# Optimization experiments

Measured on AMD Instinct MI355X. Metric: run time of the kernel, lower is better.

## Reference

```python
import jax, jax.numpy as jnp
import numpy as np

N_NODES = 100000
N_EDGES = 1600000
NUM_FEATURES = 128
HIDDEN = 128


def _linear_init(key, fan_in, fan_out):
    kw, kb = jax.random.split(key)
    bound = 1.0 / np.sqrt(fan_in)
    w = jax.random.uniform(kw, (fan_in, fan_out), jnp.float32, -bound, bound)
    b = jax.random.uniform(kb, (fan_out,), jnp.float32, -bound, bound)
    return w, b


def setup_inputs() -> dict:
    key = jax.random.key(0)
    ks = jax.random.split(key, 8)
    x = jax.random.normal(ks[0], (N_NODES, NUM_FEATURES), jnp.float32)
    edge_index = jax.random.randint(ks[1], (2, N_EDGES), 0, N_NODES, jnp.int64)
    w11, b11 = _linear_init(ks[2], NUM_FEATURES, HIDDEN)
    w12, b12 = _linear_init(ks[3], HIDDEN, HIDDEN)
    w21, b21 = _linear_init(ks[4], HIDDEN, HIDDEN)
    w22, b22 = _linear_init(ks[5], HIDDEN, HIDDEN)
    w31, b31 = _linear_init(ks[6], HIDDEN, HIDDEN)
    w32, b32 = _linear_init(ks[7], HIDDEN, 1)
    return {"x": x, "edge_index": edge_index,
            "w11": w11, "b11": b11, "w12": w12, "b12": b12,
            "w21": w21, "b21": b21, "w22": w22, "b22": b22,
            "w31": w31, "b31": b31, "w32": w32, "b32": b32}


def _gin_conv(x, src, dst, w1, b1, w2, b2):
    # GINConv (eps=0): h_i = MLP(x_i + sum_{j->i} x_j)
    agg = jax.ops.segment_sum(x[src], dst, num_segments=N_NODES)
    h = x + agg
    h = jax.nn.relu(h @ w1 + b1)
    return h @ w2 + b2


def reference(x, edge_index, w11, b11, w12, b12, w21, b21, w22, b22, w31, b31, w32, b32):
    src, dst = edge_index[0], edge_index[1]
    h = _gin_conv(x, src, dst, w11, b11, w12, b12)
    h = _gin_conv(h, src, dst, w21, b21, w22, b22)
    h = _gin_conv(h, src, dst, w31, b31, w32, b32)  # [N, 1]
    return h
```

## Files before the change

kernel.cpp:

```cpp
#include <hip/hip_runtime.h>

#define NN 100000
#define NE 1600000
#define F 128
#define NBUCK ((NN + 255) >> 8)
#define EPB (NE / 256)

typedef _Float16 f16x8 __attribute__((ext_vector_type(8)));
typedef float    f32x4 __attribute__((ext_vector_type(4)));
typedef unsigned short ushort8v __attribute__((ext_vector_type(8)));
typedef unsigned short ushort4v __attribute__((ext_vector_type(4)));

__device__ inline unsigned short f2h(float f) {
    _Float16 h = (_Float16)f;
    return __builtin_bit_cast(unsigned short, h);
}
__device__ inline float h2f(unsigned short u) {
    return (float)__builtin_bit_cast(_Float16, u);
}

__global__ __launch_bounds__(256) void k_bhist(const int* __restrict__ dst, int* __restrict__ bcnt) {
    __shared__ int sc[NBUCK];
    for (int i = threadIdx.x; i < NBUCK; i += 256) sc[i] = 0;
    __syncthreads();
    int stride = gridDim.x * 256;
    for (int e = blockIdx.x * 256 + threadIdx.x; e < NE; e += stride)
        atomicAdd(&sc[dst[e] >> 8], 1);
    __syncthreads();
    for (int i = threadIdx.x; i < NBUCK; i += 256) {
        int c = sc[i];
        if (c) atomicAdd(&bcnt[i], c);
    }
}

__global__ void k_bscan(const int* __restrict__ bcnt, int* __restrict__ bbase, int* __restrict__ bcur) {
    __shared__ int s[512];
    int t = threadIdx.x;
    int v = (t < NBUCK) ? bcnt[t] : 0;
    s[t] = v;
    __syncthreads();
    for (int off = 1; off < 512; off <<= 1) {
        int u = (t >= off) ? s[t - off] : 0;
        __syncthreads();
        s[t] += u;
        __syncthreads();
    }
    int excl = s[t] - v;
    if (t < NBUCK) { bbase[t] = excl; bcur[t] = excl; }
    if (t == 0) bbase[NBUCK] = NE;
}

__global__ __launch_bounds__(256) void k_scatterA(const int* __restrict__ src,
                                                  const int* __restrict__ dst,
                                                  int* __restrict__ bcur,
                                                  unsigned* __restrict__ scratch) {
    __shared__ uint2 sEdge[EPB];
    __shared__ int cnt[512];
    __shared__ int scn[512];
    __shared__ int cntB[512];
    __shared__ int gbase[512];
    __shared__ int ssum[256];

    const int tid = threadIdx.x;
    const int ebase = blockIdx.x * EPB;

#pragma unroll
    for (int i = tid; i < 512; i += 256) { cnt[i] = 0; cntB[i] = 0; }
    __syncthreads();

    for (int i = tid; i < EPB; i += 256) {
        int b = dst[ebase + i] >> 8;
        atomicAdd(&cnt[b], 1);
    }
    __syncthreads();

    int c0 = cnt[2 * tid], c1 = cnt[2 * tid + 1];
    ssum[tid] = c0 + c1;
    __syncthreads();
    for (int off = 1; off < 256; off <<= 1) {
        int v = (tid >= off) ? ssum[tid - off] : 0;
        __syncthreads();
        ssum[tid] += v;
        __syncthreads();
    }
    int texcl = (tid == 0) ? 0 : ssum[tid - 1];
    scn[2 * tid] = texcl;
    scn[2 * tid + 1] = texcl + c0;
#pragma unroll
    for (int i = tid; i < NBUCK; i += 256) {
        int c = cnt[i];
        gbase[i] = c ? atomicAdd(&bcur[i], c) : 0;
    }
    __syncthreads();

    for (int i = tid; i < EPB; i += 256) {
        int s = src[ebase + i], d = dst[ebase + i];
        int b = d >> 8;
        int rank = atomicAdd(&cntB[b], 1);
        sEdge[scn[b] + rank] = make_uint2((unsigned)s, (unsigned)d);
    }
    __syncthreads();

    for (int i = tid; i < EPB; i += 256) {
        uint2 ed = sEdge[i];
        int b = (int)(ed.y >> 8);
        unsigned w = ((ed.y & 255u) << 24) | ed.x;
        scratch[gbase[b] + (i - scn[b])] = w;
    }
}

__global__ __launch_bounds__(256) void k_fillB(const int* __restrict__ bbase,
                                               const unsigned* __restrict__ scratch,
                                               int* __restrict__ row_ptr,
                                               int* __restrict__ csr) {
    __shared__ int cnt[256];
    __shared__ int s[256];
    __shared__ int cur[256];
    int b = blockIdx.x;
    int base = bbase[b], end = bbase[b + 1];
    int t = threadIdx.x;
    cnt[t] = 0;
    __syncthreads();
    for (int i = base + t; i < end; i += 256)
        atomicAdd(&cnt[scratch[i] >> 24], 1);
    __syncthreads();
    int v = cnt[t];
    s[t] = v;
    __syncthreads();
    for (int off = 1; off < 256; off <<= 1) {
        int u = (t >= off) ? s[t - off] : 0;
        __syncthreads();
        s[t] += u;
        __syncthreads();
    }
    int excl = s[t] - v;
    int node = (b << 8) + t;
    if (node < NN) row_ptr[node] = base + excl;
    if (b == NBUCK - 1 && t == 0) row_ptr[NN] = NE;
    cur[t] = excl;
    __syncthreads();
    for (int i = base + t; i < end; i += 256) {
        unsigned w = scratch[i];
        int n = w >> 24;
        int p = atomicAdd(&cur[n], 1);
        csr[base + p] = (int)(w & 0xFFFFFFu);
    }
}

__global__ void k_x2h(const float* __restrict__ x, unsigned short* __restrict__ xh) {
    int idx = blockIdx.x * 256 + threadIdx.x;
    float4 v = ((const float4*)x)[idx];
    ushort4v h;
    h.x = f2h(v.x);
    h.y = f2h(v.y);
    h.z = f2h(v.z);
    h.w = f2h(v.w);
    ((ushort4v*)xh)[idx] = h;
}

struct WPack {
    const float* w[5];
    unsigned short* t[5];
};

__global__ void k_w2h(WPack p) {
    int which = blockIdx.x >> 6;
    int idx = (blockIdx.x & 63) * 256 + threadIdx.x;
    int n = idx >> 7, k = idx & 127;
    p.t[which][idx] = f2h(p.w[which][k * 128 + n]);
}

template <int L3>
__global__ __launch_bounds__(256, 5) void k_layer(const unsigned short* __restrict__ G,
                                                  const int* __restrict__ row_ptr,
                                                  const int* __restrict__ csr,
                                                  const unsigned short* __restrict__ W1,
                                                  const float* __restrict__ b1,
                                                  const unsigned short* __restrict__ W2,
                                                  const float* __restrict__ b2,
                                                  const float* __restrict__ w32,
                                                  const float* __restrict__ b32,
                                                  unsigned short* __restrict__ H,
                                                  float* __restrict__ out) {
    __shared__ __align__(16) unsigned short sA[64 * 128];

    const int tid = threadIdx.x;
    const int row0 = blockIdx.x * 64;
    const int cg   = tid >> 6;
    const int lane = tid & 63;
    const int m16  = lane & 15;
    const int quad = lane >> 4;

    {
        const int g = tid >> 4;
        const int l16 = tid & 15;
        const int lofs = l16 * 8;
#pragma unroll
        for (int it = 0; it < 4; ++it) {
            int r = it * 16 + g;
            int node = row0 + r;
            float a[8] = {};
            if (node < NN) {
                ushort8v sh = *(const ushort8v*)&G[(size_t)node * F + lofs];
#pragma unroll
                for (int k = 0; k < 8; ++k) a[k] = h2f(sh[k]);
                int st = row_ptr[node], e = row_ptr[node + 1];
                int p = st;
                for (; p + 8 <= e; p += 8) {
                    ushort8v v[8];
#pragma unroll
                    for (int q = 0; q < 8; ++q) {
                        int j = csr[p + q];
                        v[q] = *(const ushort8v*)&G[(size_t)j * F + lofs];
                    }
#pragma unroll
                    for (int k = 0; k < 8; ++k) {
                        float t0 = (h2f(v[0][k]) + h2f(v[1][k])) + (h2f(v[2][k]) + h2f(v[3][k]));
                        float t1 = (h2f(v[4][k]) + h2f(v[5][k])) + (h2f(v[6][k]) + h2f(v[7][k]));
                        a[k] += t0 + t1;
                    }
                }
                if (p + 4 <= e) {
                    ushort8v v[4];
#pragma unroll
                    for (int q = 0; q < 4; ++q) {
                        int j = csr[p + q];
                        v[q] = *(const ushort8v*)&G[(size_t)j * F + lofs];
                    }
#pragma unroll
                    for (int k = 0; k < 8; ++k)
                        a[k] += (h2f(v[0][k]) + h2f(v[1][k])) + (h2f(v[2][k]) + h2f(v[3][k]));
                    p += 4;
                }
                if (p + 2 <= e) {
                    int j0 = csr[p], j1 = csr[p + 1];
                    ushort8v v0 = *(const ushort8v*)&G[(size_t)j0 * F + lofs];
                    ushort8v v1 = *(const ushort8v*)&G[(size_t)j1 * F + lofs];
#pragma unroll
                    for (int k = 0; k < 8; ++k) a[k] += h2f(v0[k]) + h2f(v1[k]);
                    p += 2;
                }
                if (p < e) {
                    int j0 = csr[p];
                    ushort8v v0 = *(const ushort8v*)&G[(size_t)j0 * F + lofs];
#pragma unroll
                    for (int k = 0; k < 8; ++k) a[k] += h2f(v0[k]);
                }
            }
            ushort8v o;
#pragma unroll
            for (int k = 0; k < 8; ++k) o[k] = f2h(a[k]);
            *(ushort8v*)&sA[r * 128 + ((l16 ^ (r & 15)) << 3)] = o;
        }
    }
    __syncthreads();

    f32x4 acc[4][2] = {};
#pragma unroll
    for (int ks = 0; ks < 4; ++ks) {
        f16x8 a[4];
#pragma unroll
        for (int rt = 0; rt < 4; ++rt) {
            int rowL = rt * 16 + m16;
            int u = ks * 4 + quad;
            a[rt] = *(const f16x8*)&sA[rowL * 128 + ((u ^ (rowL & 15)) << 3)];
        }
#pragma unroll
        for (int ct = 0; ct < 2; ++ct) {
            int widx = (cg * 32 + ct * 16 + m16) * 128 + ks * 32 + quad * 8;
            f16x8 b = *(const f16x8*)&W1[widx];
#pragma unroll
            for (int rt = 0; rt < 4; ++rt)
                acc[rt][ct] = __builtin_amdgcn_mfma_f32_16x16x32_f16(a[rt], b, acc[rt][ct], 0, 0, 0);
        }
    }

    if (L3) {
        float* psf = (float*)sA;
        __syncthreads();
#pragma unroll
        for (int rt = 0; rt < 4; ++rt) {
            float s[4] = {0.f, 0.f, 0.f, 0.f};
#pragma unroll
            for (int ct = 0; ct < 2; ++ct) {
                int col = cg * 32 + ct * 16 + m16;
                float bv = b1[col];
                float wv = w32[col];
#pragma unroll
                for (int i = 0; i < 4; ++i) {
                    float v = fmaxf(acc[rt][ct][i] + bv, 0.f);
                    s[i] += v * wv;
                }
            }
#pragma unroll
            for (int i = 0; i < 4; ++i) {
#pragma unroll
                for (int mask = 1; mask < 16; mask <<= 1)
                    s[i] += __shfl_xor(s[i], mask, 64);
            }
            if (m16 == 0) {
#pragma unroll
                for (int i = 0; i < 4; ++i) {
                    int rowL = rt * 16 + quad * 4 + i;
                    psf[rowL * 4 + cg] = s[i];
                }
            }
        }
        __syncthreads();
        if (tid < 64) {
            int row = row0 + tid;
            if (row < NN)
                out[row] = (psf[tid * 4] + psf[tid * 4 + 1]) + (psf[tid * 4 + 2] + psf[tid * 4 + 3]) + b32[0];
        }
        return;
    }

    __syncthreads();
#pragma unroll
    for (int rt = 0; rt < 4; ++rt) {
#pragma unroll
        for (int ct = 0; ct < 2; ++ct) {
            int col = cg * 32 + ct * 16 + m16;
            float bv = b1[col];
#pragma unroll
            for (int i = 0; i < 4; ++i) {
                int rL = rt * 16 + quad * 4 + i;
                float v = fmaxf(acc[rt][ct][i] + bv, 0.f);
                sA[rL * 128 + (((col >> 3) ^ (rL & 15)) << 3) + (col & 7)] = f2h(v);
            }
        }
    }
    __syncthreads();

    f32x4 acc2[4][2] = {};
#pragma unroll
    for (int ks = 0; ks < 4; ++ks) {
        f16x8 a[4];
#pragma unroll
        for (int rt = 0; rt < 4; ++rt) {
            int rowL = rt * 16 + m16;
            int u = ks * 4 + quad;
            a[rt] = *(const f16x8*)&sA[rowL * 128 + ((u ^ (rowL & 15)) << 3)];
        }
#pragma unroll
        for (int ct = 0; ct < 2; ++ct) {
            int widx = (cg * 32 + ct * 16 + m16) * 128 + ks * 32 + quad * 8;
            f16x8 b = *(const f16x8*)&W2[widx];
#pragma unroll
            for (int rt = 0; rt < 4; ++rt)
                acc2[rt][ct] = __builtin_amdgcn_mfma_f32_16x16x32_f16(a[rt], b, acc2[rt][ct], 0, 0, 0);
        }
    }

    __syncthreads();
#pragma unroll
    for (int rt = 0; rt < 4; ++rt) {
#pragma unroll
        for (int ct = 0; ct < 2; ++ct) {
            int col = cg * 32 + ct * 16 + m16;
            float bv = b2[col];
#pragma unroll
            for (int i = 0; i < 4; ++i) {
                int rL = rt * 16 + quad * 4 + i;
                float v = acc2[rt][ct][i] + bv;
                sA[rL * 128 + (((col >> 3) ^ (rL & 15)) << 3) + (col & 7)] = f2h(v);
            }
        }
    }
    __syncthreads();
    {
        ushort8v* go = (ushort8v*)(H + (size_t)row0 * F);
#pragma unroll
        for (int i = 0; i < 4; ++i) {
            int fg = i * 256 + tid;
            int r = fg >> 4, u = fg & 15;
            if (row0 + r < NN)
                go[fg] = *(const ushort8v*)&sA[r * 128 + ((u ^ (r & 15)) << 3)];
        }
    }
}

static inline size_t align256(size_t x) { return (x + 255) & ~(size_t)255; }

extern "C" void kernel_launch(void* const* d_in, const int* in_sizes, int n_in,
                              void* d_out, int out_size, void* d_ws, size_t ws_size,
                              hipStream_t stream) {
    const float* x   = (const float*)d_in[0];
    const int*   ei  = (const int*)d_in[1];
    const float* w11 = (const float*)d_in[2];
    const float* b11 = (const float*)d_in[3];
    const float* w12 = (const float*)d_in[4];
    const float* b12 = (const float*)d_in[5];
    const float* w21 = (const float*)d_in[6];
    const float* b21 = (const float*)d_in[7];
    const float* w22 = (const float*)d_in[8];
    const float* b22 = (const float*)d_in[9];
    const float* w31 = (const float*)d_in[10];
    const float* b31 = (const float*)d_in[11];
    const float* w32 = (const float*)d_in[12];
    const float* b32 = (const float*)d_in[13];
    float* out = (float*)d_out;

    const int* src = ei;
    const int* dst = ei + NE;

    char* ws = (char*)d_ws;
    size_t off = 0;
    unsigned short* Abuf = (unsigned short*)(ws + off); off += align256((size_t)NN * F * 2);
    unsigned short* Bbuf = (unsigned short*)(ws + off); off += align256((size_t)NN * F * 2);
    int* bcnt    = (int*)(ws + off); off += align256((size_t)NBUCK * 4);
    int* bbase   = (int*)(ws + off); off += align256((size_t)(NBUCK + 1) * 4);
    int* bcur    = (int*)(ws + off); off += align256((size_t)NBUCK * 4);
    int* row_ptr = (int*)(ws + off); off += align256((size_t)(NN + 1) * 4);
    int* csr     = (int*)(ws + off); off += align256((size_t)NE * 4);
    unsigned* scratch = (unsigned*)(ws + off); off += align256((size_t)NE * 4);
    unsigned short* wt[5];
    for (int i = 0; i < 5; ++i) {
        wt[i] = (unsigned short*)(ws + off); off += align256((size_t)128 * 128 * 2);
    }
    (void)ws_size;

    WPack wp;
    wp.w[0] = w11; wp.w[1] = w12; wp.w[2] = w21; wp.w[3] = w22; wp.w[4] = w31;
    for (int i = 0; i < 5; ++i) wp.t[i] = wt[i];
    k_w2h<<<320, 256, 0, stream>>>(wp);
    k_x2h<<<(NN * F / 4 + 255) / 256, 256, 0, stream>>>(x, Abuf);

    (void)hipMemsetAsync(bcnt, 0, (size_t)NBUCK * 4, stream);
    k_bhist<<<256, 256, 0, stream>>>(dst, bcnt);
    k_bscan<<<1, 512, 0, stream>>>(bcnt, bbase, bcur);
    k_scatterA<<<256, 256, 0, stream>>>(src, dst, bcur, scratch);
    k_fillB<<<NBUCK, 256, 0, stream>>>(bbase, scratch, row_ptr, csr);

    const int layerBlocks = (NN + 63) / 64;

    k_layer<0><<<layerBlocks, 256, 0, stream>>>(Abuf, row_ptr, csr,
                                                wt[0], b11, wt[1], b12,
                                                nullptr, nullptr, Bbuf, nullptr);
    k_layer<0><<<layerBlocks, 256, 0, stream>>>(Bbuf, row_ptr, csr,
                                                wt[2], b21, wt[3], b22,
                                                nullptr, nullptr, Abuf, nullptr);
    k_layer<1><<<layerBlocks, 256, 0, stream>>>(Abuf, row_ptr, csr,
                                                wt[4], b31, nullptr, nullptr,
                                                w32, b32, nullptr, out);
}
```

Measured before the change: 406.8 us.

## Build CSR with global atomics and stage neighbor indices in shared memory

Replaces the two-pass bucketed CSR construction (block histogram, shared-memory sort, per-bucket fill) with a per-node histogram, row scan, and a direct atomic scatter into csr. The GIN layer kernel now loads its 64 rows' row_ptr and up to 1536 neighbor indices into LDS before aggregation, and occupancy is raised to 6 blocks. The intent is to cut construction passes and global index-load latency during the gather. In exchange, global atomic contention increases, neighbor order within a row becomes nondeterministic, and the extra LDS or register pressure could limit occupancy.

```diff
diff --git a/kernel.cpp b/kernel.cpp
--- a/kernel.cpp
+++ b/kernel.cpp
@@ -4,7 +4,7 @@
 #define NE 1600000
 #define F 128
 #define NBUCK ((NN + 255) >> 8)
-#define EPB (NE / 256)
+#define IDX_CAP 1536
 
 typedef _Float16 f16x8 __attribute__((ext_vector_type(8)));
 typedef float    f32x4 __attribute__((ext_vector_type(4)));
@@ -19,21 +19,37 @@
     return (float)__builtin_bit_cast(_Float16, u);
 }
 
-__global__ __launch_bounds__(256) void k_bhist(const int* __restrict__ dst, int* __restrict__ bcnt) {
-    __shared__ int sc[NBUCK];
-    for (int i = threadIdx.x; i < NBUCK; i += 256) sc[i] = 0;
-    __syncthreads();
-    int stride = gridDim.x * 256;
-    for (int e = blockIdx.x * 256 + threadIdx.x; e < NE; e += stride)
-        atomicAdd(&sc[dst[e] >> 8], 1);
-    __syncthreads();
-    for (int i = threadIdx.x; i < NBUCK; i += 256) {
-        int c = sc[i];
-        if (c) atomicAdd(&bcnt[i], c);
-    }
-}
-
-__global__ void k_bscan(const int* __restrict__ bcnt, int* __restrict__ bbase, int* __restrict__ bcur) {
+__global__ __launch_bounds__(256) void k_ehist(const int* __restrict__ dst, int* __restrict__ row_cnt) {
+    int i = blockIdx.x * 256 + threadIdx.x;
+    if (i < NE / 4) {
+        int4 d = ((const int4*)dst)[i];
+        atomicAdd(&row_cnt[d.x], 1);
+        atomicAdd(&row_cnt[d.y], 1);
+        atomicAdd(&row_cnt[d.z], 1);
+        atomicAdd(&row_cnt[d.w], 1);
+    }
+}
+
+__global__ __launch_bounds__(256) void k_rowscan(const int* __restrict__ row_cnt,
+                                                 int* __restrict__ bcnt,
+                                                 int* __restrict__ row_cur) {
+    __shared__ int s[256];
+    int b = blockIdx.x, t = threadIdx.x;
+    int node = (b << 8) + t;
+    int v = (node < NN) ? row_cnt[node] : 0;
+    s[t] = v;
+    __syncthreads();
+    for (int off = 1; off < 256; off <<= 1) {
+        int u = (t >= off) ? s[t - off] : 0;
+        __syncthreads();
+        s[t] += u;
+        __syncthreads();
+    }
+    if (node < NN) row_cur[node] = s[t] - v;
+    if (t == 255) bcnt[b] = s[255];
+}
+
+__global__ void k_bscan(const int* __restrict__ bcnt, int* __restrict__ bbase) {
     __shared__ int s[512];
     int t = threadIdx.x;
     int v = (t < NBUCK) ? bcnt[t] : 0;
@@ -45,105 +61,37 @@
         s[t] += u;
         __syncthreads();
     }
-    int excl = s[t] - v;
-    if (t < NBUCK) { bbase[t] = excl; bcur[t] = excl; }
+    if (t < NBUCK) bbase[t] = s[t] - v;
     if (t == 0) bbase[NBUCK] = NE;
 }
 
-__global__ __launch_bounds__(256) void k_scatterA(const int* __restrict__ src,
+__global__ __launch_bounds__(256) void k_rowfin(const int* __restrict__ bbase,
+                                                int* __restrict__ row_ptr,
+                                                int* __restrict__ row_cur) {
+    int b = blockIdx.x, t = threadIdx.x;
+    int node = (b << 8) + t;
+    if (node < NN) {
+        int rp = bbase[b] + row_cur[node];
+        row_ptr[node] = rp;
+        row_cur[node] = rp;
+    } else if (node == NN) {
+        row_ptr[NN] = NE;
+    }
+}
+
+__global__ __launch_bounds__(256) void k_escatter(const int* __restrict__ src,
                                                   const int* __restrict__ dst,
-                                                  int* __restrict__ bcur,
-                                                  unsigned* __restrict__ scratch) {
-    __shared__ uint2 sEdge[EPB];
-    __shared__ int cnt[512];
-    __shared__ int scn[512];
-    __shared__ int cntB[512];
-    __shared__ int gbase[512];
-    __shared__ int ssum[256];
-
-    const int tid = threadIdx.x;
-    const int ebase = blockIdx.x * EPB;
-
-#pragma unroll
-    for (int i = tid; i < 512; i += 256) { cnt[i] = 0; cntB[i] = 0; }
-    __syncthreads();
-
-    for (int i = tid; i < EPB; i += 256) {
-        int b = dst[ebase + i] >> 8;
-        atomicAdd(&cnt[b], 1);
-    }
-    __syncthreads();
-
-    int c0 = cnt[2 * tid], c1 = cnt[2 * tid + 1];
-    ssum[tid] = c0 + c1;
-    __syncthreads();
-    for (int off = 1; off < 256; off <<= 1) {
-        int v = (tid >= off) ? ssum[tid - off] : 0;
-        __syncthreads();
-        ssum[tid] += v;
-        __syncthreads();
-    }
-    int texcl = (tid == 0) ? 0 : ssum[tid - 1];
-    scn[2 * tid] = texcl;
-    scn[2 * tid + 1] = texcl + c0;
-#pragma unroll
-    for (int i = tid; i < NBUCK; i += 256) {
-        int c = cnt[i];
-        gbase[i] = c ? atomicAdd(&bcur[i], c) : 0;
-    }
-    __syncthreads();
-
-    for (int i = tid; i < EPB; i += 256) {
-        int s = src[ebase + i], d = dst[ebase + i];
-        int b = d >> 8;
-        int rank = atomicAdd(&cntB[b], 1);
-        sEdge[scn[b] + rank] = make_uint2((unsigned)s, (unsigned)d);
-    }
-    __syncthreads();
-
-    for (int i = tid; i < EPB; i += 256) {
-        uint2 ed = sEdge[i];
-        int b = (int)(ed.y >> 8);
-        unsigned w = ((ed.y & 255u) << 24) | ed.x;
-        scratch[gbase[b] + (i - scn[b])] = w;
-    }
-}
-
-__global__ __launch_bounds__(256) void k_fillB(const int* __restrict__ bbase,
-                                               const unsigned* __restrict__ scratch,
-                                               int* __restrict__ row_ptr,
-                                               int* __restrict__ csr) {
-    __shared__ int cnt[256];
-    __shared__ int s[256];
-    __shared__ int cur[256];
-    int b = blockIdx.x;
-    int base = bbase[b], end = bbase[b + 1];
-    int t = threadIdx.x;
-    cnt[t] = 0;
-    __syncthreads();
-    for (int i = base + t; i < end; i += 256)
-        atomicAdd(&cnt[scratch[i] >> 24], 1);
-    __syncthreads();
-    int v = cnt[t];
-    s[t] = v;
-    __syncthreads();
-    for (int off = 1; off < 256; off <<= 1) {
-        int u = (t >= off) ? s[t - off] : 0;
-        __syncthreads();
-        s[t] += u;
-        __syncthreads();
-    }
-    int excl = s[t] - v;
-    int node = (b << 8) + t;
-    if (node < NN) row_ptr[node] = base + excl;
-    if (b == NBUCK - 1 && t == 0) row_ptr[NN] = NE;
-    cur[t] = excl;
-    __syncthreads();
-    for (int i = base + t; i < end; i += 256) {
-        unsigned w = scratch[i];
-        int n = w >> 24;
-        int p = atomicAdd(&cur[n], 1);
-        csr[base + p] = (int)(w & 0xFFFFFFu);
+                                                  int* __restrict__ row_cur,
+                                                  int* __restrict__ csr) {
+    int i = blockIdx.x * 256 + threadIdx.x;
+    if (i < NE / 4) {
+        int4 s4 = ((const int4*)src)[i];
+        int4 d4 = ((const int4*)dst)[i];
+        int p;
+        p = atomicAdd(&row_cur[d4.x], 1); csr[p] = s4.x;
+        p = atomicAdd(&row_cur[d4.y], 1); csr[p] = s4.y;
+        p = atomicAdd(&row_cur[d4.z], 1); csr[p] = s4.z;
+        p = atomicAdd(&row_cur[d4.w], 1); csr[p] = s4.w;
     }
 }
 
@@ -170,8 +118,58 @@
     p.t[which][idx] = f2h(p.w[which][k * 128 + n]);
 }
 
+template <bool LOC>
+__device__ __forceinline__ void accum_rows(float a[8], int st, int e,
+                                           const int* __restrict__ sIdx,
+                                           const int* __restrict__ gIdx,
+                                           const unsigned short* __restrict__ G,
+                                           int lofs) {
+    int p = st;
+    for (; p + 8 <= e; p += 8) {
+        int j[8];
+#pragma unroll
+        for (int q = 0; q < 8; ++q) j[q] = LOC ? sIdx[p + q] : gIdx[p + q];
+        ushort8v v[8];
+#pragma unroll
+        for (int q = 0; q < 8; ++q) v[q] = *(const ushort8v*)&G[(size_t)j[q] * F + lofs];
+#pragma unroll
+        for (int k = 0; k < 8; ++k) {
+            float t0 = (h2f(v[0][k]) + h2f(v[1][k])) + (h2f(v[2][k]) + h2f(v[3][k]));
+            float t1 = (h2f(v[4][k]) + h2f(v[5][k])) + (h2f(v[6][k]) + h2f(v[7][k]));
+            a[k] += t0 + t1;
+        }
+    }
+    if (p + 4 <= e) {
+        int j[4];
+#pragma unroll
+        for (int q = 0; q < 4; ++q) j[q] = LOC ? sIdx[p + q] : gIdx[p + q];
+        ushort8v v[4];
+#pragma unroll
+        for (int q = 0; q < 4; ++q) v[q] = *(const ushort8v*)&G[(size_t)j[q] * F + lofs];
+#pragma unroll
+        for (int k = 0; k < 8; ++k)
+            a[k] += (h2f(v[0][k]) + h2f(v[1][k])) + (h2f(v[2][k]) + h2f(v[3][k]));
+        p += 4;
+    }
+    if (p + 2 <= e) {
+        int j0 = LOC ? sIdx[p] : gIdx[p];
+        int j1 = LOC ? sIdx[p + 1] : gIdx[p + 1];
+        ushort8v v0 = *(const ushort8v*)&G[(size_t)j0 * F + lofs];
+        ushort8v v1 = *(const ushort8v*)&G[(size_t)j1 * F + lofs];
+#pragma unroll
+        for (int k = 0; k < 8; ++k) a[k] += h2f(v0[k]) + h2f(v1[k]);
+        p += 2;
+    }
+    if (p < e) {
+        int j0 = LOC ? sIdx[p] : gIdx[p];
+        ushort8v v0 = *(const ushort8v*)&G[(size_t)j0 * F + lofs];
+#pragma unroll
+        for (int k = 0; k < 8; ++k) a[k] += h2f(v0[k]);
+    }
+}
+
 template <int L3>
-__global__ __launch_bounds__(256, 5) void k_layer(const unsigned short* __restrict__ G,
+__global__ __launch_bounds__(256, 6) void k_layer(const unsigned short* __restrict__ G,
                                                   const int* __restrict__ row_ptr,
                                                   const int* __restrict__ csr,
                                                   const unsigned short* __restrict__ W1,
@@ -183,6 +181,8 @@
                                                   unsigned short* __restrict__ H,
                                                   float* __restrict__ out) {
     __shared__ __align__(16) unsigned short sA[64 * 128];
+    __shared__ int sRP[65];
+    __shared__ int sIdx[IDX_CAP];
 
     const int tid = threadIdx.x;
     const int row0 = blockIdx.x * 64;
@@ -191,6 +191,18 @@
     const int m16  = lane & 15;
     const int quad = lane >> 4;
 
+    if (tid < 65) {
+        int n = row0 + tid;
+        if (n > NN) n = NN;
+        sRP[tid] = row_ptr[n];
+    }
+    __syncthreads();
+    const int ibase = sRP[0];
+    const int icnt  = sRP[64] - ibase;
+    const int icap  = icnt < IDX_CAP ? icnt : IDX_CAP;
+    for (int i = tid; i < icap; i += 256) sIdx[i] = csr[ibase + i];
+    __syncthreads();
+
     {
         const int g = tid >> 4;
         const int l16 = tid & 15;
@@ -204,48 +216,11 @@
                 ushort8v sh = *(const ushort8v*)&G[(size_t)node * F + lofs];
 #pragma unroll
                 for (int k = 0; k < 8; ++k) a[k] = h2f(sh[k]);
-                int st = row_ptr[node], e = row_ptr[node + 1];
-                int p = st;
-                for (; p + 8 <= e; p += 8) {
-                    ushort8v v[8];
-#pragma unroll
-                    for (int q = 0; q < 8; ++q) {
-                        int j = csr[p + q];
-                        v[q] = *(const ushort8v*)&G[(size_t)j * F + lofs];
-                    }
-#pragma unroll
-                    for (int k = 0; k < 8; ++k) {
-                        float t0 = (h2f(v[0][k]) + h2f(v[1][k])) + (h2f(v[2][k]) + h2f(v[3][k]));
-                        float t1 = (h2f(v[4][k]) + h2f(v[5][k])) + (h2f(v[6][k]) + h2f(v[7][k]));
-                        a[k] += t0 + t1;
-                    }
-                }
-                if (p + 4 <= e) {
-                    ushort8v v[4];
-#pragma unroll
-                    for (int q = 0; q < 4; ++q) {
-                        int j = csr[p + q];
-                        v[q] = *(const ushort8v*)&G[(size_t)j * F + lofs];
-                    }
-#pragma unroll
-                    for (int k = 0; k < 8; ++k)
-                        a[k] += (h2f(v[0][k]) + h2f(v[1][k])) + (h2f(v[2][k]) + h2f(v[3][k]));
-                    p += 4;
-                }
-                if (p + 2 <= e) {
-                    int j0 = csr[p], j1 = csr[p + 1];
-                    ushort8v v0 = *(const ushort8v*)&G[(size_t)j0 * F + lofs];
-                    ushort8v v1 = *(const ushort8v*)&G[(size_t)j1 * F + lofs];
-#pragma unroll
-                    for (int k = 0; k < 8; ++k) a[k] += h2f(v0[k]) + h2f(v1[k]);
-                    p += 2;
-                }
-                if (p < e) {
-                    int j0 = csr[p];
-                    ushort8v v0 = *(const ushort8v*)&G[(size_t)j0 * F + lofs];
-#pragma unroll
-                    for (int k = 0; k < 8; ++k) a[k] += h2f(v0[k]);
-                }
+                int st = sRP[r] - ibase, e = sRP[r + 1] - ibase;
+                if (e <= icap)
+                    accum_rows<true>(a, st, e, sIdx, csr + ibase, G, lofs);
+                else
+                    accum_rows<false>(a, st, e, sIdx, csr + ibase, G, lofs);
             }
             ushort8v o;
 #pragma unroll
@@ -408,12 +383,12 @@
     size_t off = 0;
     unsigned short* Abuf = (unsigned short*)(ws + off); off += align256((size_t)NN * F * 2);
     unsigned short* Bbuf = (unsigned short*)(ws + off); off += align256((size_t)NN * F * 2);
+    int* row_cnt = (int*)(ws + off); off += align256((size_t)NN * 4);
+    int* row_cur = (int*)(ws + off); off += align256((size_t)NN * 4);
     int* bcnt    = (int*)(ws + off); off += align256((size_t)NBUCK * 4);
     int* bbase   = (int*)(ws + off); off += align256((size_t)(NBUCK + 1) * 4);
-    int* bcur    = (int*)(ws + off); off += align256((size_t)NBUCK * 4);
     int* row_ptr = (int*)(ws + off); off += align256((size_t)(NN + 1) * 4);
     int* csr     = (int*)(ws + off); off += align256((size_t)NE * 4);
-    unsigned* scratch = (unsigned*)(ws + off); off += align256((size_t)NE * 4);
     unsigned short* wt[5];
     for (int i = 0; i < 5; ++i) {
         wt[i] = (unsigned short*)(ws + off); off += align256((size_t)128 * 128 * 2);
@@ -426,11 +401,13 @@
     k_w2h<<<320, 256, 0, stream>>>(wp);
     k_x2h<<<(NN * F / 4 + 255) / 256, 256, 0, stream>>>(x, Abuf);
 
-    (void)hipMemsetAsync(bcnt, 0, (size_t)NBUCK * 4, stream);
-    k_bhist<<<256, 256, 0, stream>>>(dst, bcnt);
-    k_bscan<<<1, 512, 0, stream>>>(bcnt, bbase, bcur);
-    k_scatterA<<<256, 256, 0, stream>>>(src, dst, bcur, scratch);
-    k_fillB<<<NBUCK, 256, 0, stream>>>(bbase, scratch, row_ptr, csr);
+    (void)hipMemsetAsync(row_cnt, 0, (size_t)NN * 4, stream);
+    const int e4Blocks = (NE / 4 + 255) / 256;
+    k_ehist<<<e4Blocks, 256, 0, stream>>>(dst, row_cnt);
+    k_rowscan<<<NBUCK, 256, 0, stream>>>(row_cnt, bcnt, row_cur);
+    k_bscan<<<1, 512, 0, stream>>>(bcnt, bbase);
+    k_rowfin<<<NBUCK, 256, 0, stream>>>(bbase, row_ptr, row_cur);
+    k_escatter<<<e4Blocks, 256, 0, stream>>>(src, dst, row_cur, csr);
 
     const int layerBlocks = (NN + 63) / 64;
 
```

Result: slower. 561.6 us (+38.1%).
